# Kernel optimization log

Hardware: AMD Instinct MI355X
Metric: run time of the kernel (lower is better)

## Reference

```python
import jax, jax.numpy as jnp
import numpy as np

BSZ, SEQ, D, NHEAD, NLAYER, DFF, NQ = 4, 48, 256, 2, 2, 2048, 512
LN_EPS = 1e-5
NEG = jnp.float32(-1e30)


def _layernorm(x, w, b):
    m = jnp.mean(x, axis=-1, keepdims=True)
    v = jnp.mean((x - m) ** 2, axis=-1, keepdims=True)
    return (x - m) / jnp.sqrt(v + LN_EPS) * w + b


def _span_max(x):
    # Cumulative span max: span[b,s,e] = max(x[b,s:e+1]) for e>=s, else 0.
    B, S, H = x.shape
    padded = jnp.concatenate([x, jnp.full((B, S, H), NEG, x.dtype)], axis=1)  # [B,2S,H]

    def step(tmp, i):
        shifted = jax.lax.dynamic_slice(padded, (0, i, 0), (B, S, H))  # x shifted left by i, padded with -inf
        tmp = jnp.maximum(tmp, shifted)  # tmp[b,s] = max(x[b,s:s+i+1])
        return tmp, tmp

    _, ys = jax.lax.scan(step, jnp.full((B, S, H), NEG, x.dtype), jnp.arange(S))
    # ys: [width, B, start, H]; span[b,s,e] = ys[e-s, b, s]
    si = jnp.arange(S)[:, None]
    ei = jnp.arange(S)[None, :]
    w = jnp.clip(ei - si, 0, S - 1)
    span = ys[w, :, jnp.broadcast_to(si, (S, S))]  # [S_start, S_end, B, H]
    span = jnp.where((ei >= si)[:, :, None, None], span, 0.0)
    return span.transpose(2, 0, 1, 3)  # [B,S,S,H]


def _mha(x, wi, bi, wo, bo, kpm):
    # x: [B,T,D]; kpm: [B,T] bool, True = masked key
    B, T, Dm = x.shape
    hd = Dm // NHEAD
    qkv = x @ wi.T + bi
    q, k, v = jnp.split(qkv, 3, axis=-1)
    rs = lambda a: a.reshape(B, T, NHEAD, hd).transpose(0, 2, 1, 3)
    q, k, v = rs(q), rs(k), rs(v)
    scores = jnp.einsum('bhqd,bhkd->bhqk', q, k) * (1.0 / np.sqrt(hd))
    scores = jnp.where(kpm[:, None, None, :], -1e9, scores)
    p = jax.nn.softmax(scores, axis=-1)
    o = jnp.einsum('bhqk,bhkd->bhqd', p, v).transpose(0, 2, 1, 3).reshape(B, T, Dm)
    return o @ wo.T + bo


def _encoder(x, kpm, iw, ib, ow, ob, l1w, l1b, l2w, l2b, f1w, f1b, f2w, f2b, fw, fb):
    # Post-norm torch TransformerEncoder (eval mode, relu, no dropout)
    for l in range(NLAYER):
        a = _mha(x, iw[l], ib[l], ow[l], ob[l], kpm)
        x = _layernorm(x + a, l1w[l], l1b[l])
        f = jax.nn.relu(x @ f1w[l].T + f1b[l]) @ f2w[l].T + f2b[l]
        x = _layernorm(x + f, l2w[l], l2b[l])
    return _layernorm(x, fw, fb)


def _forward(enc, iw, ib, ow, ob, l1w, l1b, l2w, l2b, f1w, f1b, f2w, f2b, fw, fb, s1, e1, qb, s2, e2):
    span = _span_max(enc)  # [B,S,S,D]
    idx = jnp.arange(SEQ)
    kpm2d = idx[None, :] < idx[:, None]  # [start,end]: True where end < start
    kpm = jnp.broadcast_to(kpm2d.reshape(1, SEQ * SEQ), (BSZ, SEQ * SEQ))
    out = _encoder(span.reshape(BSZ, SEQ * SEQ, D), kpm, iw, ib, ow, ob, l1w, l1b, l2w, l2b, f1w, f1b, f2w, f2b, fw, fb)
    out = out.reshape(BSZ, SEQ, SEQ, D)
    res1 = out[qb, s1, e1]
    res2 = out[qb, s2, e2]
    return res1, res2


def setup_inputs() -> dict:
    key = jax.random.key(0)
    ks = jax.random.split(key, 16)
    sc = 0.02
    enc = jax.random.normal(ks[0], (BSZ, SEQ, D), jnp.float32)
    inp = {
        'encoded_input': enc,
        'in_proj_w': jax.random.normal(ks[1], (NLAYER, 3 * D, D), jnp.float32) * sc,
        'in_proj_b': jnp.zeros((NLAYER, 3 * D), jnp.float32),
        'out_proj_w': jax.random.normal(ks[2], (NLAYER, D, D), jnp.float32) * sc,
        'out_proj_b': jnp.zeros((NLAYER, D), jnp.float32),
        'ln1_w': jnp.ones((NLAYER, D), jnp.float32),
        'ln1_b': jnp.zeros((NLAYER, D), jnp.float32),
        'ln2_w': jnp.ones((NLAYER, D), jnp.float32),
        'ln2_b': jnp.zeros((NLAYER, D), jnp.float32),
        'ff1_w': jax.random.normal(ks[3], (NLAYER, DFF, D), jnp.float32) * sc,
        'ff1_b': jnp.zeros((NLAYER, DFF), jnp.float32),
        'ff2_w': jax.random.normal(ks[4], (NLAYER, D, DFF), jnp.float32) * sc,
        'ff2_b': jnp.zeros((NLAYER, D), jnp.float32),
        'fln_w': jnp.ones((D,), jnp.float32),
        'fln_b': jnp.zeros((D,), jnp.float32),
    }
    s1 = jax.random.randint(ks[5], (NQ,), 0, SEQ)
    e1 = jnp.minimum(s1 + jax.random.randint(ks[6], (NQ,), 0, SEQ), SEQ - 1)
    s2 = jax.random.randint(ks[7], (NQ,), 0, SEQ)
    e2 = jnp.minimum(s2 + jax.random.randint(ks[8], (NQ,), 0, SEQ), SEQ - 1)
    inp['start_ids_1'] = s1
    inp['end_ids_1'] = e1
    inp['query_batch_idx'] = jax.random.randint(ks[9], (NQ,), 0, BSZ)
    inp['start_ids_2'] = s2
    inp['end_ids_2'] = e2
    return inp


def reference(encoded_input, in_proj_w, in_proj_b, out_proj_w, out_proj_b, ln1_w, ln1_b, ln2_w, ln2_b, ff1_w, ff1_b, ff2_w, ff2_b, fln_w, fln_b, start_ids_1, end_ids_1, query_batch_idx, start_ids_2, end_ids_2):
    return _forward(encoded_input, in_proj_w, in_proj_b, out_proj_w, out_proj_b, ln1_w, ln1_b, ln2_w, ln2_b, ff1_w, ff1_b, ff2_w, ff2_b, fln_w, fln_b, start_ids_1, end_ids_1, query_batch_idx, start_ids_2, end_ids_2)
```

## Files before the change

kernel.cpp:

```cpp
#include <hip/hip_runtime.h>
#include <hip/hip_bf16.h>

#define BSZ 4
#define SEQ 48
#define DMODEL 256
#define NHEAD 2
#define HD 128
#define NLAYERS 2
#define DFF_C 2048
#define NQ_C 512
#define NV 1176
#define NTOT (BSZ * NV)
#define NVP 1216
#define KSPLIT 5
#define SCALE 0.088388347648318447f

typedef unsigned short u16;
typedef __attribute__((ext_vector_type(8))) short bf16x8;
typedef __attribute__((ext_vector_type(4))) float f32x4;

__device__ inline u16 f2b(float f) {
    __hip_bfloat16 h = __float2bfloat16(f);
    return *reinterpret_cast<u16*>(&h);
}
__device__ inline void storeval(float* p, float v) { *p = v; }
__device__ inline void storeval(u16* p, float v) { *p = f2b(v); }

__global__ __launch_bounds__(256) void span_kernel(const float* __restrict__ enc,
                                                   float* __restrict__ X,
                                                   u16* __restrict__ Xb) {
    int i = blockIdx.x, b = blockIdx.y, h = threadIdx.x;
    int tb = i * SEQ - (i * (i - 1)) / 2 - i;
    float run = -1e30f;
    for (int j = i; j < SEQ; ++j) {
        run = fmaxf(run, enc[((size_t)b * SEQ + j) * DMODEL + h]);
        size_t idx = ((size_t)b * NV + tb + j) * DMODEL + h;
        X[idx] = run;
        Xb[idx] = f2b(run);
    }
}

__global__ __launch_bounds__(256) void castall_kernel(
    const float* __restrict__ iw, const float* __restrict__ ow,
    const float* __restrict__ f1w, const float* __restrict__ f2w,
    u16* __restrict__ iwb, u16* __restrict__ owb,
    u16* __restrict__ f1wb, u16* __restrict__ f2wb) {
    int i = blockIdx.x * 256 + threadIdx.x;
    const float* src;
    u16* dst;
    int off;
    if (i < 98304)       { src = iw;  dst = iwb;  off = i; }
    else if (i < 131072) { src = ow;  dst = owb;  off = i - 98304; }
    else if (i < 393216) { src = f1w; dst = f1wb; off = i - 131072; }
    else                 { src = f2w; dst = f2wb; off = i - 393216; }
    float4 v = *(const float4*)(src + (size_t)off * 4);
    *(ushort4*)(dst + (size_t)off * 4) =
        make_ushort4(f2b(v.x), f2b(v.y), f2b(v.z), f2b(v.w));
}

template <typename OutT, bool RELU, bool ATOMIC>
__global__ __launch_bounds__(256) void mm_kernel(
    const u16* __restrict__ A, const u16* __restrict__ W,
    const float* __restrict__ bias, const float* __restrict__ Res,
    OutT* __restrict__ C, int N, int K, int lda, int ldw, int ldc,
    float alpha, int WV, int KC) {
    __shared__ u16 As[64][40];
    __shared__ u16 Ws[64][40];
    const float4 fz = make_float4(0.f, 0.f, 0.f, 0.f);
    int ks = blockIdx.z;
    int kb = ks * KC, ke = min(K, kb + KC);
    int p0 = blockIdx.x * 64, n0 = blockIdx.y * 64;
    int tid = threadIdx.x, lane = tid & 63, w = tid >> 6;
    int col_l = lane & 15, quad = lane >> 4;
    f32x4 acc[4] = {};
    for (int k0 = kb; k0 < ke; k0 += 32) {
        int r = tid >> 2, seg = (tid & 3) * 8;
        {
            int gn = n0 + r;
            float4 av = fz;
            if (gn < N) av = *(const float4*)(A + (size_t)gn * lda + k0 + seg);
            *(float4*)&As[r][seg] = av;
        }
        {
            int gp = p0 + r;
            float4 wv = fz;
            if (gp < WV) wv = *(const float4*)(W + (size_t)gp * ldw + k0 + seg);
            *(float4*)&Ws[r][seg] = wv;
        }
        __syncthreads();
        bf16x8 a = *(const bf16x8*)&As[w * 16 + col_l][quad * 8];
#pragma unroll
        for (int c = 0; c < 4; ++c) {
            bf16x8 b = *(const bf16x8*)&Ws[c * 16 + col_l][quad * 8];
            acc[c] = __builtin_amdgcn_mfma_f32_16x16x32_bf16(a, b, acc[c], 0, 0, 0);
        }
        __syncthreads();
    }
#pragma unroll
    for (int c = 0; c < 4; ++c) {
        int col = p0 + c * 16 + col_l;
        float bv = bias ? bias[col] : 0.f;
#pragma unroll
        for (int reg = 0; reg < 4; ++reg) {
            int row = n0 + w * 16 + quad * 4 + reg;
            if (row < N) {
                float v = acc[c][reg] * alpha + bv;
                if (Res) v += Res[(size_t)row * ldc + col];
                if (RELU) v = fmaxf(v, 0.f);
                if (ATOMIC) {
                    unsafeAtomicAdd((float*)&C[(size_t)row * ldc + col], v);
                } else {
                    storeval(&C[(size_t)row * ldc + col], v);
                }
            }
        }
    }
}

__global__ __launch_bounds__(256) void vtrans_kernel(const u16* __restrict__ QKVb,
                                                     u16* __restrict__ VT) {
    __shared__ u16 T[64][66];
    const float4 fz = make_float4(0.f, 0.f, 0.f, 0.f);
    int kt = blockIdx.x, dt = blockIdx.y, bh = blockIdx.z;
    int b = bh >> 1, h = bh & 1;
    size_t rb = (size_t)b * NV;
    int tid = threadIdx.x;
    {
        int r = tid >> 2, cs = (tid & 3) * 16;
        int key = kt * 64 + r;
        float4 v0 = fz, v1 = fz;
        if (key < NV) {
            const u16* vp = QKVb + (rb + key) * 768 + 2 * DMODEL + h * HD + dt * 64 + cs;
            v0 = *(const float4*)vp;
            v1 = *(const float4*)(vp + 8);
        }
        *(float4*)&T[r][cs] = v0;
        *(float4*)&T[r][cs + 8] = v1;
    }
    __syncthreads();
    {
        int dl = tid >> 2, ks2 = (tid & 3) * 16;
        u16 tmp[16];
#pragma unroll
        for (int j = 0; j < 16; ++j) tmp[j] = T[ks2 + j][dl];
        u16* dst = VT + ((size_t)bh * HD + dt * 64 + dl) * NVP + kt * 64 + ks2;
        *(float4*)dst = *(float4*)&tmp[0];
        *(float4*)(dst + 8) = *(float4*)&tmp[8];
    }
}

__global__ __launch_bounds__(256) void flash_kernel(const u16* __restrict__ QKVb,
                                                    const u16* __restrict__ VT,
                                                    float* __restrict__ Opart,
                                                    float* __restrict__ ML) {
    __shared__ u16 Ks[64][136];
    __shared__ u16 Vt[128][72];
    __shared__ u16 Ps[4][16][72];
    const float4 fz = make_float4(0.f, 0.f, 0.f, 0.f);
    int tid = threadIdx.x, lane = tid & 63, w = tid >> 6;
    int col_l = lane & 15, quad = lane >> 4;
    int bh = blockIdx.y, b = bh >> 1, h = bh & 1;
    int ks = blockIdx.z;
    int t0 = ks * 4, tcnt = min(4, 19 - t0);
    size_t rb = (size_t)b * NV;
    int q0 = blockIdx.x * 64, wq0 = q0 + w * 16;

    float4 qv[4];
    {
        int qrow = wq0 + col_l;
        if (qrow < NV) {
            const u16* qp = QKVb + (rb + qrow) * 768 + h * HD + quad * 8;
#pragma unroll
            for (int kf = 0; kf < 4; ++kf) qv[kf] = *(const float4*)(qp + kf * 32);
        } else {
#pragma unroll
            for (int kf = 0; kf < 4; ++kf) qv[kf] = fz;
        }
    }

    f32x4 oacc[8] = {};
    float m_run[4], l_run[4];
#pragma unroll
    for (int r = 0; r < 4; ++r) { m_run[r] = -1e30f; l_run[r] = 0.f; }

    for (int it = 0; it < tcnt; ++it) {
        int kt = (t0 + it) * 64;
        {
            int r = tid >> 2, seg = (tid & 3) * 32;
            int key = kt + r;
            const u16* kp = QKVb + (rb + key) * 768 + DMODEL + h * HD + seg;
#pragma unroll
            for (int t4 = 0; t4 < 4; ++t4) {
                float4 v = fz;
                if (key < NV) v = *(const float4*)(kp + t4 * 8);
                *(float4*)&Ks[r][seg + t4 * 8] = v;
            }
        }
        {
            int d = tid >> 1, half = (tid & 1) * 32;
            const u16* vp = VT + ((size_t)bh * HD + d) * NVP + kt + half;
#pragma unroll
            for (int t4 = 0; t4 < 4; ++t4)
                *(float4*)&Vt[d][half + t4 * 8] = *(const float4*)(vp + t4 * 8);
        }
        __syncthreads();

        f32x4 s[4] = {};
#pragma unroll
        for (int c = 0; c < 4; ++c)
#pragma unroll
            for (int kf = 0; kf < 4; ++kf) {
                bf16x8 kfr = *(const bf16x8*)&Ks[c * 16 + col_l][kf * 32 + quad * 8];
                s[c] = __builtin_amdgcn_mfma_f32_16x16x32_bf16(
                    *(const bf16x8*)&qv[kf], kfr, s[c], 0, 0, 0);
            }

        float pv[4][4];
#pragma unroll
        for (int c = 0; c < 4; ++c) {
            bool kvalid = (kt + c * 16 + col_l) < NV;
#pragma unroll
            for (int r = 0; r < 4; ++r)
                pv[c][r] = kvalid ? s[c][r] * SCALE : -1e30f;
        }
        float al[4];
#pragma unroll
        for (int r = 0; r < 4; ++r) {
            float mx = fmaxf(fmaxf(pv[0][r], pv[1][r]), fmaxf(pv[2][r], pv[3][r]));
#pragma unroll
            for (int off = 1; off < 16; off <<= 1)
                mx = fmaxf(mx, __shfl_xor(mx, off));
            float mn = fmaxf(m_run[r], mx);
            al[r] = __expf(m_run[r] - mn);
            m_run[r] = mn;
            float sum = 0.f;
#pragma unroll
            for (int c = 0; c < 4; ++c) {
                float p = __expf(pv[c][r] - mn);
                pv[c][r] = p;
                sum += p;
            }
#pragma unroll
            for (int off = 1; off < 16; off <<= 1) sum += __shfl_xor(sum, off);
            l_run[r] = l_run[r] * al[r] + sum;
        }
#pragma unroll
        for (int ct = 0; ct < 8; ++ct)
#pragma unroll
            for (int r = 0; r < 4; ++r) oacc[ct][r] *= al[r];

#pragma unroll
        for (int c = 0; c < 4; ++c)
#pragma unroll
            for (int r = 0; r < 4; ++r)
                Ps[w][quad * 4 + r][c * 16 + col_l] = f2b(pv[c][r]);
        bf16x8 pf0 = *(const bf16x8*)&Ps[w][col_l][quad * 8];
        bf16x8 pf1 = *(const bf16x8*)&Ps[w][col_l][32 + quad * 8];
#pragma unroll
        for (int ct = 0; ct < 8; ++ct) {
            bf16x8 v0 = *(const bf16x8*)&Vt[ct * 16 + col_l][quad * 8];
            bf16x8 v1 = *(const bf16x8*)&Vt[ct * 16 + col_l][32 + quad * 8];
            oacc[ct] = __builtin_amdgcn_mfma_f32_16x16x32_bf16(pf0, v0, oacc[ct], 0, 0, 0);
            oacc[ct] = __builtin_amdgcn_mfma_f32_16x16x32_bf16(pf1, v1, oacc[ct], 0, 0, 0);
        }
        __syncthreads();
    }

    size_t slab = (size_t)(ks * 8 + bh) * NVP;
#pragma unroll
    for (int ct = 0; ct < 8; ++ct)
#pragma unroll
        for (int r = 0; r < 4; ++r) {
            int row = wq0 + quad * 4 + r;
            Opart[(slab + row) * HD + ct * 16 + col_l] = oacc[ct][r];
        }
    if (col_l == 0) {
#pragma unroll
        for (int r = 0; r < 4; ++r) {
            int row = wq0 + quad * 4 + r;
            ML[(slab + row) * 2 + 0] = m_run[r];
            ML[(slab + row) * 2 + 1] = l_run[r];
        }
    }
}

__global__ __launch_bounds__(256) void comb_kernel(const float* __restrict__ Opart,
                                                   const float* __restrict__ ML,
                                                   u16* __restrict__ Obuf) {
    int bh = blockIdx.y, b = bh >> 1, h = bh & 1;
    int tid = threadIdx.x;
    int row = blockIdx.x * 2 + (tid >> 7);
    int d = tid & 127;
    if (row >= NV) return;
    float m[KSPLIT], l[KSPLIT];
#pragma unroll
    for (int i = 0; i < KSPLIT; ++i) {
        size_t mb = ((size_t)(i * 8 + bh) * NVP + row) * 2;
        m[i] = ML[mb];
        l[i] = ML[mb + 1];
    }
    float M = m[0];
#pragma unroll
    for (int i = 1; i < KSPLIT; ++i) M = fmaxf(M, m[i]);
    float wsum = 0.f, o = 0.f;
#pragma unroll
    for (int i = 0; i < KSPLIT; ++i) {
        float wi = __expf(m[i] - M);
        wsum += l[i] * wi;
        o += Opart[((size_t)(i * 8 + bh) * NVP + row) * HD + d] * wi;
    }
    Obuf[((size_t)b * NV + row) * DMODEL + h * HD + d] = f2b(o / wsum);
}

__global__ __launch_bounds__(256) void ln_kernel(const float* __restrict__ Xin,
                                                 const float* __restrict__ Res,
                                                 const float* __restrict__ w,
                                                 const float* __restrict__ bb,
                                                 float* __restrict__ Y,
                                                 u16* __restrict__ Yb,
                                                 const float* __restrict__ fb2,
                                                 float* __restrict__ A2out) {
    int r = blockIdx.x, d = threadIdx.x;
    size_t idx = (size_t)r * DMODEL + d;
    float v = Xin[idx];
    if (Res) v += Res[idx];
    float s1 = v, s2 = v * v;
#pragma unroll
    for (int off = 32; off > 0; off >>= 1) {
        s1 += __shfl_down(s1, off);
        s2 += __shfl_down(s2, off);
    }
    __shared__ float ps1[4], ps2[4];
    int wid = d >> 6, lane = d & 63;
    if (lane == 0) { ps1[wid] = s1; ps2[wid] = s2; }
    __syncthreads();
    if (d == 0) {
        ps1[0] = ps1[0] + ps1[1] + ps1[2] + ps1[3];
        ps2[0] = ps2[0] + ps2[1] + ps2[2] + ps2[3];
    }
    __syncthreads();
    float mean = ps1[0] * (1.f / DMODEL);
    float var = ps2[0] * (1.f / DMODEL) - mean * mean;
    float o = (v - mean) * rsqrtf(var + 1e-5f) * w[d] + bb[d];
    Y[idx] = o;
    Yb[idx] = f2b(o);
    if (A2out) A2out[idx] = o + fb2[d];
}

__global__ __launch_bounds__(256) void gather_kernel(const float* __restrict__ Xf,
                                                     const int* __restrict__ s1,
                                                     const int* __restrict__ e1,
                                                     const int* __restrict__ qb,
                                                     const int* __restrict__ s2,
                                                     const int* __restrict__ e2,
                                                     float* __restrict__ out) {
    int q = blockIdx.x, which = blockIdx.y, d = threadIdx.x;
    int s = which ? s2[q] : s1[q];
    int e = which ? e2[q] : e1[q];
    int b = qb[q];
    int t = s * SEQ - (s * (s - 1)) / 2 + (e - s);
    if (t < 0) t = 0;
    if (t >= NV) t = NV - 1;
    out[((size_t)which * NQ_C + q) * DMODEL + d] = Xf[((size_t)b * NV + t) * DMODEL + d];
}

extern "C" void kernel_launch(void* const* d_in, const int* in_sizes, int n_in,
                              void* d_out, int out_size, void* d_ws, size_t ws_size,
                              hipStream_t stream) {
    const float* enc = (const float*)d_in[0];
    const float* iw  = (const float*)d_in[1];
    const float* ib  = (const float*)d_in[2];
    const float* ow  = (const float*)d_in[3];
    const float* ob  = (const float*)d_in[4];
    const float* l1w = (const float*)d_in[5];
    const float* l1b = (const float*)d_in[6];
    const float* l2w = (const float*)d_in[7];
    const float* l2b = (const float*)d_in[8];
    const float* f1w = (const float*)d_in[9];
    const float* f1b = (const float*)d_in[10];
    const float* f2w = (const float*)d_in[11];
    const float* f2b_ = (const float*)d_in[12];
    const float* flw = (const float*)d_in[13];
    const float* flb = (const float*)d_in[14];
    const int* s1 = (const int*)d_in[15];
    const int* e1 = (const int*)d_in[16];
    const int* qb = (const int*)d_in[17];
    const int* s2 = (const int*)d_in[18];
    const int* e2 = (const int*)d_in[19];
    float* out = (float*)d_out;

    char* p = (char*)d_ws;
    float* X     = (float*)p;  p += (size_t)NTOT * DMODEL * 4;
    float* A2    = (float*)p;  p += (size_t)NTOT * DMODEL * 4;
    u16* Xb      = (u16*)p;    p += (size_t)NTOT * DMODEL * 2;
    u16* Obuf    = (u16*)p;    p += (size_t)NTOT * DMODEL * 2;
    u16* QKVb    = (u16*)p;    p += (size_t)NTOT * 3 * DMODEL * 2;
    u16* VT      = (u16*)p;    p += (size_t)8 * HD * NVP * 2;
    float* ML    = (float*)p;  p += (size_t)KSPLIT * 8 * NVP * 2 * 4;
    float* Opart = (float*)p;  p += (size_t)KSPLIT * 8 * NVP * HD * 4;
    u16* wb      = (u16*)p;
    u16* F1b     = (u16*)Opart;
    float* Of    = A2;

    u16* iwb  = wb;
    u16* owb  = iwb + 2 * 3 * DMODEL * DMODEL;
    u16* f1wb = owb + 2 * DMODEL * DMODEL;
    u16* f2wb = f1wb + 2 * DFF_C * DMODEL;

    castall_kernel<<<dim3(2560), 256, 0, stream>>>(iw, ow, f1w, f2w,
                                                   iwb, owb, f1wb, f2wb);
    span_kernel<<<dim3(SEQ, BSZ), 256, 0, stream>>>(enc, X, Xb);

    for (int l = 0; l < NLAYERS; ++l) {
        mm_kernel<u16, false, false><<<dim3(12, 74, 1), 256, 0, stream>>>(
            Xb, iwb + (size_t)l * 3 * DMODEL * DMODEL, ib + (size_t)l * 3 * DMODEL,
            nullptr, QKVb, NTOT, DMODEL, DMODEL, DMODEL, 3 * DMODEL, 1.f,
            3 * DMODEL, DMODEL);
        vtrans_kernel<<<dim3(19, 2, 8), 256, 0, stream>>>(QKVb, VT);
        flash_kernel<<<dim3(19, 8, KSPLIT), 256, 0, stream>>>(QKVb, VT, Opart, ML);
        comb_kernel<<<dim3(588, 8), 256, 0, stream>>>(Opart, ML, Obuf);
        mm_kernel<float, false, false><<<dim3(4, 74, 1), 256, 0, stream>>>(
            Obuf, owb + (size_t)l * DMODEL * DMODEL, ob + (size_t)l * DMODEL,
            X, A2, NTOT, DMODEL, DMODEL, DMODEL, DMODEL, 1.f, DMODEL, DMODEL);
        ln_kernel<<<dim3(NTOT), 256, 0, stream>>>(
            A2, nullptr, l1w + (size_t)l * DMODEL, l1b + (size_t)l * DMODEL,
            X, Xb, f2b_ + (size_t)l * DMODEL, A2);
        mm_kernel<u16, true, false><<<dim3(32, 74, 1), 256, 0, stream>>>(
            Xb, f1wb + (size_t)l * DFF_C * DMODEL, f1b + (size_t)l * DFF_C,
            nullptr, F1b, NTOT, DMODEL, DMODEL, DMODEL, DFF_C, 1.f, DFF_C, DMODEL);
        mm_kernel<float, false, true><<<dim3(4, 74, 4), 256, 0, stream>>>(
            F1b, f2wb + (size_t)l * DMODEL * DFF_C, nullptr, nullptr, A2,
            NTOT, DFF_C, DFF_C, DFF_C, DMODEL, 1.f, DMODEL, 512);
        ln_kernel<<<dim3(NTOT), 256, 0, stream>>>(
            A2, nullptr, l2w + (size_t)l * DMODEL, l2b + (size_t)l * DMODEL,
            X, Xb, nullptr, nullptr);
    }
    ln_kernel<<<dim3(NTOT), 256, 0, stream>>>(X, nullptr, flw, flb, Of, Xb,
                                              nullptr, nullptr);
    gather_kernel<<<dim3(NQ_C, 2), 256, 0, stream>>>(Of, s1, e1, qb, s2, e2, out);
}
```

Measured before the change: 360.5 us.

## Fuse cast/span and final LN/gather, widen GEMM K-tile, warp-per-row layernorm

Merges the weight cast and span-max kernels into one launch, and folds the final layernorm into the gather so only the gathered rows are normalized. The GEMM kernel gains a templated K-tile size (64 or 128), which halves or quarters the number of barrier-separated iterations. Layernorm switches to one wavefront per row with float4 accesses and shuffle-only reductions, removing the shared-memory reductions and barriers. Costs are more LDS per GEMM block and a little extra register pressure.

```diff
diff --git a/kernel.cpp b/kernel.cpp
--- a/kernel.cpp
+++ b/kernel.cpp
@@ -26,46 +26,48 @@
 __device__ inline void storeval(float* p, float v) { *p = v; }
 __device__ inline void storeval(u16* p, float v) { *p = f2b(v); }
 
-__global__ __launch_bounds__(256) void span_kernel(const float* __restrict__ enc,
-                                                   float* __restrict__ X,
-                                                   u16* __restrict__ Xb) {
-    int i = blockIdx.x, b = blockIdx.y, h = threadIdx.x;
-    int tb = i * SEQ - (i * (i - 1)) / 2 - i;
-    float run = -1e30f;
-    for (int j = i; j < SEQ; ++j) {
-        run = fmaxf(run, enc[((size_t)b * SEQ + j) * DMODEL + h]);
-        size_t idx = ((size_t)b * NV + tb + j) * DMODEL + h;
-        X[idx] = run;
-        Xb[idx] = f2b(run);
-    }
-}
-
-__global__ __launch_bounds__(256) void castall_kernel(
+__global__ __launch_bounds__(256) void castspan_kernel(
     const float* __restrict__ iw, const float* __restrict__ ow,
     const float* __restrict__ f1w, const float* __restrict__ f2w,
     u16* __restrict__ iwb, u16* __restrict__ owb,
-    u16* __restrict__ f1wb, u16* __restrict__ f2wb) {
-    int i = blockIdx.x * 256 + threadIdx.x;
-    const float* src;
-    u16* dst;
-    int off;
-    if (i < 98304)       { src = iw;  dst = iwb;  off = i; }
-    else if (i < 131072) { src = ow;  dst = owb;  off = i - 98304; }
-    else if (i < 393216) { src = f1w; dst = f1wb; off = i - 131072; }
-    else                 { src = f2w; dst = f2wb; off = i - 393216; }
-    float4 v = *(const float4*)(src + (size_t)off * 4);
-    *(ushort4*)(dst + (size_t)off * 4) =
-        make_ushort4(f2b(v.x), f2b(v.y), f2b(v.z), f2b(v.w));
-}
-
-template <typename OutT, bool RELU, bool ATOMIC>
+    u16* __restrict__ f1wb, u16* __restrict__ f2wb,
+    const float* __restrict__ enc, float* __restrict__ X,
+    u16* __restrict__ Xb) {
+    int bid = blockIdx.x;
+    if (bid < 2560) {
+        int i = bid * 256 + threadIdx.x;
+        const float* src;
+        u16* dst;
+        int off;
+        if (i < 98304)       { src = iw;  dst = iwb;  off = i; }
+        else if (i < 131072) { src = ow;  dst = owb;  off = i - 98304; }
+        else if (i < 393216) { src = f1w; dst = f1wb; off = i - 131072; }
+        else                 { src = f2w; dst = f2wb; off = i - 393216; }
+        float4 v = *(const float4*)(src + (size_t)off * 4);
+        *(ushort4*)(dst + (size_t)off * 4) =
+            make_ushort4(f2b(v.x), f2b(v.y), f2b(v.z), f2b(v.w));
+    } else {
+        int sb = bid - 2560;
+        int i = sb % SEQ, b = sb / SEQ, h = threadIdx.x;
+        int tb = i * SEQ - (i * (i - 1)) / 2 - i;
+        float run = -1e30f;
+        for (int j = i; j < SEQ; ++j) {
+            run = fmaxf(run, enc[((size_t)b * SEQ + j) * DMODEL + h]);
+            size_t idx = ((size_t)b * NV + tb + j) * DMODEL + h;
+            X[idx] = run;
+            Xb[idx] = f2b(run);
+        }
+    }
+}
+
+template <typename OutT, bool RELU, bool ATOMIC, int BK>
 __global__ __launch_bounds__(256) void mm_kernel(
     const u16* __restrict__ A, const u16* __restrict__ W,
     const float* __restrict__ bias, const float* __restrict__ Res,
     OutT* __restrict__ C, int N, int K, int lda, int ldw, int ldc,
     float alpha, int WV, int KC) {
-    __shared__ u16 As[64][40];
-    __shared__ u16 Ws[64][40];
+    __shared__ u16 As[64][BK + 8];
+    __shared__ u16 Ws[64][BK + 8];
     const float4 fz = make_float4(0.f, 0.f, 0.f, 0.f);
     int ks = blockIdx.z;
     int kb = ks * KC, ke = min(K, kb + KC);
@@ -73,26 +75,40 @@
     int tid = threadIdx.x, lane = tid & 63, w = tid >> 6;
     int col_l = lane & 15, quad = lane >> 4;
     f32x4 acc[4] = {};
-    for (int k0 = kb; k0 < ke; k0 += 32) {
-        int r = tid >> 2, seg = (tid & 3) * 8;
+    for (int k0 = kb; k0 < ke; k0 += BK) {
+        int r = tid >> 2, seg = (tid & 3) * (BK / 4);
         {
             int gn = n0 + r;
-            float4 av = fz;
-            if (gn < N) av = *(const float4*)(A + (size_t)gn * lda + k0 + seg);
-            *(float4*)&As[r][seg] = av;
+            const u16* ap = A + (size_t)gn * lda + k0 + seg;
+#pragma unroll
+            for (int j = 0; j < BK / 32; ++j) {
+                float4 av = fz;
+                if (gn < N) av = *(const float4*)(ap + j * 8);
+                *(float4*)&As[r][seg + j * 8] = av;
+            }
         }
         {
             int gp = p0 + r;
-            float4 wv = fz;
-            if (gp < WV) wv = *(const float4*)(W + (size_t)gp * ldw + k0 + seg);
-            *(float4*)&Ws[r][seg] = wv;
+            const u16* wp = W + (size_t)gp * ldw + k0 + seg;
+#pragma unroll
+            for (int j = 0; j < BK / 32; ++j) {
+                float4 wv = fz;
+                if (gp < WV) wv = *(const float4*)(wp + j * 8);
+                *(float4*)&Ws[r][seg + j * 8] = wv;
+            }
         }
         __syncthreads();
-        bf16x8 a = *(const bf16x8*)&As[w * 16 + col_l][quad * 8];
+        bf16x8 a[BK / 32];
+#pragma unroll
+        for (int kf = 0; kf < BK / 32; ++kf)
+            a[kf] = *(const bf16x8*)&As[w * 16 + col_l][kf * 32 + quad * 8];
 #pragma unroll
         for (int c = 0; c < 4; ++c) {
-            bf16x8 b = *(const bf16x8*)&Ws[c * 16 + col_l][quad * 8];
-            acc[c] = __builtin_amdgcn_mfma_f32_16x16x32_bf16(a, b, acc[c], 0, 0, 0);
+#pragma unroll
+            for (int kf = 0; kf < BK / 32; ++kf) {
+                bf16x8 b = *(const bf16x8*)&Ws[c * 16 + col_l][kf * 32 + quad * 8];
+                acc[c] = __builtin_amdgcn_mfma_f32_16x16x32_bf16(a[kf], b, acc[c], 0, 0, 0);
+            }
         }
         __syncthreads();
     }
@@ -313,55 +329,76 @@
 }
 
 __global__ __launch_bounds__(256) void ln_kernel(const float* __restrict__ Xin,
-                                                 const float* __restrict__ Res,
                                                  const float* __restrict__ w,
                                                  const float* __restrict__ bb,
                                                  float* __restrict__ Y,
                                                  u16* __restrict__ Yb,
                                                  const float* __restrict__ fb2,
                                                  float* __restrict__ A2out) {
-    int r = blockIdx.x, d = threadIdx.x;
-    size_t idx = (size_t)r * DMODEL + d;
-    float v = Xin[idx];
-    if (Res) v += Res[idx];
-    float s1 = v, s2 = v * v;
+    int wv = threadIdx.x >> 6, lane = threadIdx.x & 63;
+    int r = blockIdx.x * 4 + wv;
+    size_t base = (size_t)r * DMODEL + lane * 4;
+    float4 v = *(const float4*)(Xin + base);
+    float s1 = v.x + v.y + v.z + v.w;
+    float s2 = v.x * v.x + v.y * v.y + v.z * v.z + v.w * v.w;
 #pragma unroll
     for (int off = 32; off > 0; off >>= 1) {
-        s1 += __shfl_down(s1, off);
-        s2 += __shfl_down(s2, off);
-    }
-    __shared__ float ps1[4], ps2[4];
-    int wid = d >> 6, lane = d & 63;
-    if (lane == 0) { ps1[wid] = s1; ps2[wid] = s2; }
-    __syncthreads();
-    if (d == 0) {
-        ps1[0] = ps1[0] + ps1[1] + ps1[2] + ps1[3];
-        ps2[0] = ps2[0] + ps2[1] + ps2[2] + ps2[3];
-    }
-    __syncthreads();
-    float mean = ps1[0] * (1.f / DMODEL);
-    float var = ps2[0] * (1.f / DMODEL) - mean * mean;
-    float o = (v - mean) * rsqrtf(var + 1e-5f) * w[d] + bb[d];
-    Y[idx] = o;
-    Yb[idx] = f2b(o);
-    if (A2out) A2out[idx] = o + fb2[d];
-}
-
-__global__ __launch_bounds__(256) void gather_kernel(const float* __restrict__ Xf,
-                                                     const int* __restrict__ s1,
-                                                     const int* __restrict__ e1,
-                                                     const int* __restrict__ qb,
-                                                     const int* __restrict__ s2,
-                                                     const int* __restrict__ e2,
-                                                     float* __restrict__ out) {
-    int q = blockIdx.x, which = blockIdx.y, d = threadIdx.x;
+        s1 += __shfl_xor(s1, off);
+        s2 += __shfl_xor(s2, off);
+    }
+    float mean = s1 * (1.f / DMODEL);
+    float var = s2 * (1.f / DMODEL) - mean * mean;
+    float rstd = rsqrtf(var + 1e-5f);
+    float4 w4 = *(const float4*)(w + lane * 4);
+    float4 b4 = *(const float4*)(bb + lane * 4);
+    float o0 = (v.x - mean) * rstd * w4.x + b4.x;
+    float o1 = (v.y - mean) * rstd * w4.y + b4.y;
+    float o2 = (v.z - mean) * rstd * w4.z + b4.z;
+    float o3 = (v.w - mean) * rstd * w4.w + b4.w;
+    *(float4*)(Y + base) = make_float4(o0, o1, o2, o3);
+    *(ushort4*)(Yb + base) = make_ushort4(f2b(o0), f2b(o1), f2b(o2), f2b(o3));
+    if (A2out) {
+        float4 f4 = *(const float4*)(fb2 + lane * 4);
+        *(float4*)(A2out + base) = make_float4(o0 + f4.x, o1 + f4.y, o2 + f4.z, o3 + f4.w);
+    }
+}
+
+__global__ __launch_bounds__(64) void gatherln_kernel(const float* __restrict__ X,
+                                                      const float* __restrict__ fw,
+                                                      const float* __restrict__ fb,
+                                                      const int* __restrict__ s1,
+                                                      const int* __restrict__ e1,
+                                                      const int* __restrict__ qb,
+                                                      const int* __restrict__ s2,
+                                                      const int* __restrict__ e2,
+                                                      float* __restrict__ out) {
+    int q = blockIdx.x, which = blockIdx.y, lane = threadIdx.x;
     int s = which ? s2[q] : s1[q];
     int e = which ? e2[q] : e1[q];
     int b = qb[q];
     int t = s * SEQ - (s * (s - 1)) / 2 + (e - s);
     if (t < 0) t = 0;
     if (t >= NV) t = NV - 1;
-    out[((size_t)which * NQ_C + q) * DMODEL + d] = Xf[((size_t)b * NV + t) * DMODEL + d];
+    size_t base = ((size_t)b * NV + t) * DMODEL + lane * 4;
+    float4 v = *(const float4*)(X + base);
+    float s1v = v.x + v.y + v.z + v.w;
+    float s2v = v.x * v.x + v.y * v.y + v.z * v.z + v.w * v.w;
+#pragma unroll
+    for (int off = 32; off > 0; off >>= 1) {
+        s1v += __shfl_xor(s1v, off);
+        s2v += __shfl_xor(s2v, off);
+    }
+    float mean = s1v * (1.f / DMODEL);
+    float var = s2v * (1.f / DMODEL) - mean * mean;
+    float rstd = rsqrtf(var + 1e-5f);
+    float4 w4 = *(const float4*)(fw + lane * 4);
+    float4 b4 = *(const float4*)(fb + lane * 4);
+    float o0 = (v.x - mean) * rstd * w4.x + b4.x;
+    float o1 = (v.y - mean) * rstd * w4.y + b4.y;
+    float o2 = (v.z - mean) * rstd * w4.z + b4.z;
+    float o3 = (v.w - mean) * rstd * w4.w + b4.w;
+    *(float4*)(out + ((size_t)which * NQ_C + q) * DMODEL + lane * 4) =
+        make_float4(o0, o1, o2, o3);
 }
 
 extern "C" void kernel_launch(void* const* d_in, const int* in_sizes, int n_in,
@@ -400,42 +437,40 @@
     float* Opart = (float*)p;  p += (size_t)KSPLIT * 8 * NVP * HD * 4;
     u16* wb      = (u16*)p;
     u16* F1b     = (u16*)Opart;
-    float* Of    = A2;
 
     u16* iwb  = wb;
     u16* owb  = iwb + 2 * 3 * DMODEL * DMODEL;
     u16* f1wb = owb + 2 * DMODEL * DMODEL;
     u16* f2wb = f1wb + 2 * DFF_C * DMODEL;
 
-    castall_kernel<<<dim3(2560), 256, 0, stream>>>(iw, ow, f1w, f2w,
-                                                   iwb, owb, f1wb, f2wb);
-    span_kernel<<<dim3(SEQ, BSZ), 256, 0, stream>>>(enc, X, Xb);
+    castspan_kernel<<<dim3(2752), 256, 0, stream>>>(iw, ow, f1w, f2w,
+                                                    iwb, owb, f1wb, f2wb,
+                                                    enc, X, Xb);
 
     for (int l = 0; l < NLAYERS; ++l) {
-        mm_kernel<u16, false, false><<<dim3(12, 74, 1), 256, 0, stream>>>(
+        mm_kernel<u16, false, false, 64><<<dim3(12, 74, 1), 256, 0, stream>>>(
             Xb, iwb + (size_t)l * 3 * DMODEL * DMODEL, ib + (size_t)l * 3 * DMODEL,
             nullptr, QKVb, NTOT, DMODEL, DMODEL, DMODEL, 3 * DMODEL, 1.f,
             3 * DMODEL, DMODEL);
         vtrans_kernel<<<dim3(19, 2, 8), 256, 0, stream>>>(QKVb, VT);
         flash_kernel<<<dim3(19, 8, KSPLIT), 256, 0, stream>>>(QKVb, VT, Opart, ML);
         comb_kernel<<<dim3(588, 8), 256, 0, stream>>>(Opart, ML, Obuf);
-        mm_kernel<float, false, false><<<dim3(4, 74, 1), 256, 0, stream>>>(
+        mm_kernel<float, false, false, 64><<<dim3(4, 74, 1), 256, 0, stream>>>(
             Obuf, owb + (size_t)l * DMODEL * DMODEL, ob + (size_t)l * DMODEL,
             X, A2, NTOT, DMODEL, DMODEL, DMODEL, DMODEL, 1.f, DMODEL, DMODEL);
-        ln_kernel<<<dim3(NTOT), 256, 0, stream>>>(
-            A2, nullptr, l1w + (size_t)l * DMODEL, l1b + (size_t)l * DMODEL,
+        ln_kernel<<<dim3(NTOT / 4), 256, 0, stream>>>(
+            A2, l1w + (size_t)l * DMODEL, l1b + (size_t)l * DMODEL,
             X, Xb, f2b_ + (size_t)l * DMODEL, A2);
-        mm_kernel<u16, true, false><<<dim3(32, 74, 1), 256, 0, stream>>>(
+        mm_kernel<u16, true, false, 64><<<dim3(32, 74, 1), 256, 0, stream>>>(
             Xb, f1wb + (size_t)l * DFF_C * DMODEL, f1b + (size_t)l * DFF_C,
             nullptr, F1b, NTOT, DMODEL, DMODEL, DMODEL, DFF_C, 1.f, DFF_C, DMODEL);
-        mm_kernel<float, false, true><<<dim3(4, 74, 4), 256, 0, stream>>>(
+        mm_kernel<float, false, true, 128><<<dim3(4, 74, 4), 256, 0, stream>>>(
             F1b, f2wb + (size_t)l * DMODEL * DFF_C, nullptr, nullptr, A2,
             NTOT, DFF_C, DFF_C, DFF_C, DMODEL, 1.f, DMODEL, 512);
-        ln_kernel<<<dim3(NTOT), 256, 0, stream>>>(
-            A2, nullptr, l2w + (size_t)l * DMODEL, l2b + (size_t)l * DMODEL,
+        ln_kernel<<<dim3(NTOT / 4), 256, 0, stream>>>(
+            A2, l2w + (size_t)l * DMODEL, l2b + (size_t)l * DMODEL,
             X, Xb, nullptr, nullptr);
     }
-    ln_kernel<<<dim3(NTOT), 256, 0, stream>>>(X, nullptr, flw, flb, Of, Xb,
-                                              nullptr, nullptr);
-    gather_kernel<<<dim3(NQ_C, 2), 256, 0, stream>>>(Of, s1, e1, qb, s2, e2, out);
-}
+    gatherln_kernel<<<dim3(NQ_C, 2), 64, 0, stream>>>(X, flw, flb,
+                                                      s1, e1, qb, s2, e2, out);
+}
```

After: 352.8 us. 2.2% less time.
